# Kernel optimization log

Hardware: AMD Instinct MI355X
Metric: run time of the kernel (lower is better)

Reference implementation:

```python
import jax, jax.numpy as jnp
import numpy as np

N_ATOMS = 16384
N_EDGES = 524288
N_MOL = 256
A = 4            # num_pseudo_species
S = 4            # len(unique_numbers)
NMAX = 10        # radial basis size
NSPH = 9         # (l_max+1)^2 with l_max=2
Q = A * NMAX
NL = 3           # l_max+1
F = Q * Q * NL   # 4800 power-spectrum features
CUTOFF = 5.0
AVG_ATOMS = 64.0
SCALE = 1.0
H1, H2 = 512, 512


def _sph_l012(u):
    # real spherical harmonics l=0,1,2 on unit vectors u [E,3] -> [E,9]
    x, y, z = u[:, 0], u[:, 1], u[:, 2]
    c1 = 0.4886025119029199
    c2 = 1.0925484305920792
    return jnp.stack([
        jnp.full_like(x, 0.28209479177387814),
        c1 * y, c1 * z, c1 * x,
        c2 * x * y, c2 * y * z,
        0.31539156525252005 * (3.0 * z * z - 1.0),
        c2 * x * z,
        0.5462742152960396 * (x * x - y * y),
    ], axis=-1)


def _forward(positions, cells, edge_offsets, U, gamma, beta, W1, W2, W3, Wc,
             numbers, edge_indices, batch):
    send, recv = edge_indices[0], edge_indices[1]
    cell_e = cells[batch[send]]                                  # [E,3,3]
    rvec = positions[recv] - positions[send] + jnp.einsum('ek,ekl->el', edge_offsets, cell_e)
    r = jnp.sqrt(jnp.sum(rvec * rvec, axis=-1) + 1e-12)          # [E]
    rhat = rvec / r[:, None]
    fc = 0.5 * (jnp.cos(jnp.pi * r / CUTOFF) + 1.0) * (r < CUTOFF)
    mu = jnp.linspace(0.0, CUTOFF, NMAX)
    sig = CUTOFF / NMAX
    R = jnp.exp(-((r[:, None] - mu) ** 2) / (2.0 * sig * sig)) * fc[:, None]  # [E,NMAX]
    Y = _sph_l012(rhat)                                          # [E,9]
    RY = jnp.einsum('en,ek->enk', R, Y)                          # [E,NMAX,9]
    w = U[:, numbers[send]]                                      # [A,E] pseudo-species mix of neighbor species
    # spherical expansion per atom: c[i,a,n,lm]
    c = jnp.stack([jax.ops.segment_sum(w[a][:, None, None] * RY, recv, num_segments=N_ATOMS)
                   for a in range(A)], axis=1)                   # [N,A,NMAX,9]
    c = c.reshape(N_ATOMS, Q, NSPH)
    # power spectrum: contract over m within each l block, normalize by sqrt(2l+1)
    lblocks = [(0, 1, 1.0), (1, 4, 3.0), (4, 9, 5.0)]
    ps = jnp.stack([jnp.einsum('iqm,ipm->iqp', c[:, :, a:b], c[:, :, a:b]) / jnp.sqrt(nl)
                    for a, b, nl in lblocks], axis=-1).reshape(N_ATOMS, F)
    # layer norm
    mean = ps.mean(axis=-1, keepdims=True)
    var = ps.var(axis=-1, keepdims=True)
    x = (ps - mean) / jnp.sqrt(var + 1e-5) * gamma + beta

    def contract(x, W):
        # species-indexed contraction: per-species weight via combination matrix U
        Wsp = jnp.einsum('as,aio->sio', U, W)                    # [S,in,out]
        out = jnp.zeros((x.shape[0], W.shape[-1]), x.dtype)
        for s in range(S):                                       # small fixed species set
            out = out + jnp.where((numbers == s)[:, None], x @ Wsp[s], 0.0)
        return out

    x = jax.nn.silu(contract(x, W1))
    x = jax.nn.silu(contract(x, W2))
    x = contract(x, W3)                                          # [N,1]
    e = jax.ops.segment_sum(x, batch, num_segments=N_MOL)        # [M,1]
    e = e / jnp.sqrt(float(A)) / AVG_ATOMS
    comp = jax.ops.segment_sum(jax.nn.one_hot(numbers, S, dtype=x.dtype), batch, num_segments=N_MOL)
    return e * SCALE + comp @ Wc.T


def setup_inputs() -> dict:
    key = jax.random.key(0)
    ks = jax.random.split(key, 10)
    positions = jax.random.normal(ks[0], (N_ATOMS, 3), dtype=jnp.float32)
    cells = jnp.zeros((N_MOL, 3, 3), dtype=jnp.float32)
    numbers = jax.random.randint(ks[1], (N_ATOMS,), 0, S)
    edge_indices = jax.random.randint(ks[2], (2, N_EDGES), 0, N_ATOMS)
    edge_offsets = jnp.zeros((N_EDGES, 3), dtype=jnp.float32)
    batch = jnp.sort(jax.random.randint(ks[3], (N_ATOMS,), 0, N_MOL))
    U = jax.random.normal(ks[4], (A, S), dtype=jnp.float32) * 0.5
    gamma = jnp.ones((F,), dtype=jnp.float32)
    beta = jnp.zeros((F,), dtype=jnp.float32)
    W1 = jax.random.normal(ks[5], (A, F, H1), dtype=jnp.float32) / np.sqrt(F)
    W2 = jax.random.normal(ks[6], (A, H1, H2), dtype=jnp.float32) / np.sqrt(H1)
    W3 = jax.random.normal(ks[7], (A, H2, 1), dtype=jnp.float32) / np.sqrt(H2)
    Wc = jax.random.normal(ks[8], (1, S), dtype=jnp.float32) * 0.1
    return {"positions": positions, "cells": cells, "numbers": numbers,
            "edge_indices": edge_indices, "edge_offsets": edge_offsets, "batch": batch,
            "U": U, "gamma": gamma, "beta": beta, "W1": W1, "W2": W2, "W3": W3, "Wc": Wc}


def reference(positions, cells, numbers, edge_indices, edge_offsets, batch,
              U, gamma, beta, W1, W2, W3, Wc):
    return _forward(positions, cells, edge_offsets, U, gamma, beta, W1, W2, W3, Wc,
                    numbers, edge_indices, batch)
```

## Files before the change

kernel.cpp:

```cpp
#include <hip/hip_runtime.h>

#define NA   16384
#define NE   524288
#define NM   256
#define FF   4800
#define FR   2496
#define FL   832
#define NPAIR 820
#define HH   512
#define NMX  10
#define NSPH 9

typedef __bf16 bf16x8 __attribute__((ext_vector_type(8)));
typedef float  f32x4  __attribute__((ext_vector_type(4)));
typedef unsigned short u16x8 __attribute__((ext_vector_type(8)));

__device__ inline unsigned short f2bf(float x){
  unsigned int u = __builtin_bit_cast(unsigned int, x);
  u += 0x7fffu + ((u >> 16) & 1u);
  return (unsigned short)(u >> 16);
}
__device__ inline float bf2f(unsigned short h){
  unsigned int u = ((unsigned int)h) << 16;
  return __builtin_bit_cast(float, u);
}
__device__ inline void atomic_add_f(float* p, float v){
  __hip_atomic_fetch_add(p, v, __ATOMIC_RELAXED, __HIP_MEMORY_SCOPE_AGENT);
}
__device__ inline void gload16(const void* g, void* l){
  __builtin_amdgcn_global_load_lds(
      (const __attribute__((address_space(1))) unsigned int*)g,
      (__attribute__((address_space(3))) unsigned int*)l, 16, 0, 0);
}
__device__ inline float silu(float x){ return x / (1.f + __expf(-x)); }

__device__ inline void build_qp(unsigned short* qp, int tid){
  if (tid < 40){
    int q = tid;
    int m0 = q * 40 - (q * (q - 1)) / 2;
    for (int p = q; p < 40; p++) qp[m0 + p - q] = (unsigned short)((q << 8) | p);
  }
}

__device__ inline int block_scan_excl(int v, int tid, int* lds){
  int lane = tid & 63, w = tid >> 6;
  int x = v;
  #pragma unroll
  for (int d = 1; d < 64; d <<= 1){
    int y = __shfl_up(x, d, 64);
    if (lane >= d) x += y;
  }
  if (lane == 63) lds[w] = x;
  __syncthreads();
  int wsum = 0;
  for (int i = 0; i < w; i++) wsum += lds[i];
  return wsum + x - v;
}

__global__ __launch_bounds__(256) void k_hist(const int* __restrict__ ei,
                                              const int* __restrict__ numbers,
                                              int* __restrict__ cnt64k){
  int e = blockIdx.x * 256 + threadIdx.x;
  if (e < NE){
    int key = ei[NE + e] * 4 + numbers[ei[e]];
    atomicAdd(&cnt64k[key], 1);
  }
}

__global__ __launch_bounds__(256) void k_scanA(const int* __restrict__ cnt64k,
                                               int* __restrict__ bsum){
  __shared__ int lds[4];
  int tid = threadIdx.x;
  int v = cnt64k[blockIdx.x * 256 + tid];
  int lane = tid & 63;
  #pragma unroll
  for (int m = 32; m; m >>= 1) v += __shfl_xor(v, m, 64);
  if (lane == 0) lds[tid >> 6] = v;
  __syncthreads();
  if (tid == 0) bsum[blockIdx.x] = lds[0] + lds[1] + lds[2] + lds[3];
}

__global__ __launch_bounds__(256) void k_scanB(const int* __restrict__ bsum,
                                               int* __restrict__ boff, int* __restrict__ starts){
  __shared__ int lds[4];
  int tid = threadIdx.x;
  int v = bsum[tid];
  int e = block_scan_excl(v, tid, lds);
  boff[tid] = e;
  if (tid == 0) starts[65536] = NE;
}

__global__ __launch_bounds__(256) void k_scanC(const int* __restrict__ cnt64k,
                                               const int* __restrict__ boff,
                                               int* __restrict__ starts, int* __restrict__ cursor){
  __shared__ int lds[4];
  int tid = threadIdx.x;
  int bin = blockIdx.x * 256 + tid;
  int v = cnt64k[bin];
  int e = block_scan_excl(v, tid, lds) + boff[blockIdx.x];
  starts[bin] = e;
  cursor[bin] = e;
}

__global__ __launch_bounds__(256) void k_sortperm(const int* __restrict__ ei,
                                                  const int* __restrict__ numbers,
                                                  int* __restrict__ cursor, int* __restrict__ perm){
  int e = blockIdx.x * 256 + threadIdx.x;
  if (e < NE){
    int key = ei[NE + e] * 4 + numbers[ei[e]];
    int p = atomicAdd(&cursor[key], 1);
    perm[p] = e;
  }
}

__global__ __launch_bounds__(256) void k_acount(const int* __restrict__ numbers,
                                                int* __restrict__ bhist){
  __shared__ int h[4];
  int tid = threadIdx.x;
  if (tid < 4) h[tid] = 0;
  __syncthreads();
  atomicAdd(&h[numbers[blockIdx.x * 256 + tid]], 1);
  __syncthreads();
  if (tid < 4) bhist[blockIdx.x * 4 + tid] = h[tid];
}

__global__ void k_aoffs(const int* __restrict__ bhist, int* __restrict__ boffs,
                        int* __restrict__ ints){
  if (threadIdx.x == 0){
    int* cnt = ints; int* offs = ints + 8;
    int tot[4] = {0,0,0,0};
    for (int b = 0; b < 64; b++)
      for (int s = 0; s < 4; s++) tot[s] += bhist[b*4 + s];
    int o = 0;
    for (int s = 0; s < 4; s++){ cnt[s] = tot[s]; offs[s] = o; o += tot[s]; }
    offs[4] = o;
    int run[4];
    for (int s = 0; s < 4; s++) run[s] = offs[s];
    for (int b = 0; b < 64; b++)
      for (int s = 0; s < 4; s++){ boffs[b*4 + s] = run[s]; run[s] += bhist[b*4 + s]; }
  }
}

__global__ __launch_bounds__(256) void k_aplace(const int* __restrict__ numbers,
                                                const int* __restrict__ boffs,
                                                int* __restrict__ list){
  __shared__ int ws[4][4];
  int tid = threadIdx.x, w = tid >> 6, lane = tid & 63;
  int i = blockIdx.x * 256 + tid;
  int sp = numbers[i];
  int rank = 0;
  #pragma unroll
  for (int s = 0; s < 4; s++){
    unsigned long long m = __ballot(sp == s);
    if (s == sp) rank = __popcll(m & (((unsigned long long)1 << lane) - 1));
    if (lane == 0) ws[w][s] = __popcll(m);
  }
  __syncthreads();
  int pre = 0;
  for (int w2 = 0; w2 < w; w2++) pre += ws[w2][sp];
  list[boffs[blockIdx.x * 4 + sp] + pre + rank] = i;
}

__global__ __launch_bounds__(384) void k_atom(
    const float* __restrict__ pos, const float* __restrict__ cells,
    const int* __restrict__ ei, const float* __restrict__ eoff,
    const int* __restrict__ batch, const int* __restrict__ startsK,
    const int* __restrict__ perm, const float* __restrict__ U,
    unsigned short* __restrict__ ps, float* __restrict__ stats)
{
  __shared__ float Rl[64][NMX];
  __shared__ float Yl[64][NSPH];
  __shared__ float csr[360];
  __shared__ float cl[360];
  __shared__ float red[16];
  __shared__ float ul[16];
  __shared__ unsigned short qp[NPAIR];
  int atom = blockIdx.x;
  int tid = threadIdx.x;
  if (tid < 16) ul[tid] = U[tid];
  build_qp(qp, tid);
  int e0 = startsK[atom * 4], e1 = startsK[atom * 4 + 4];
  float px = pos[atom*3+0], py = pos[atom*3+1], pz = pos[atom*3+2];
  int sp = tid / 90, n = (tid % 90) / 9, k = tid % 9;
  int aS = 0, aE = 0;
  if (tid < 360){ aS = startsK[atom * 4 + sp]; aE = startsK[atom * 4 + sp + 1]; }
  float acc = 0.f;
  for (int base = e0; base < e1; base += 64){
    int nch = min(64, e1 - base);
    if (tid < nch){
      int e = perm[base + tid];
      int snd = ei[e];
      const float* C = cells + (size_t)batch[snd] * 9;
      float o0 = eoff[e*3+0], o1 = eoff[e*3+1], o2 = eoff[e*3+2];
      float rx = px - pos[snd*3+0] + o0*C[0] + o1*C[3] + o2*C[6];
      float ry = py - pos[snd*3+1] + o0*C[1] + o1*C[4] + o2*C[7];
      float rz = pz - pos[snd*3+2] + o0*C[2] + o1*C[5] + o2*C[8];
      float r = sqrtf(rx*rx + ry*ry + rz*rz + 1e-12f);
      float inv = 1.f / r;
      float hx = rx*inv, hy = ry*inv, hz = rz*inv;
      float fc = (r < 5.f) ? (0.5f * (__cosf(r * 0.6283185307179586f) + 1.f)) : 0.f;
      #pragma unroll
      for (int nn = 0; nn < NMX; nn++){
        float d = r - (5.f/9.f) * (float)nn;
        Rl[tid][nn] = __expf(-2.f * d * d) * fc;
      }
      Yl[tid][0] = 0.28209479177387814f;
      Yl[tid][1] = 0.4886025119029199f * hy;
      Yl[tid][2] = 0.4886025119029199f * hz;
      Yl[tid][3] = 0.4886025119029199f * hx;
      Yl[tid][4] = 1.0925484305920792f * hx * hy;
      Yl[tid][5] = 1.0925484305920792f * hy * hz;
      Yl[tid][6] = 0.31539156525252005f * (3.f * hz * hz - 1.f);
      Yl[tid][7] = 1.0925484305920792f * hx * hz;
      Yl[tid][8] = 0.5462742152960396f * (hx * hx - hy * hy);
    }
    __syncthreads();
    if (tid < 360){
      int lo2 = max(aS, base), hi2 = min(aE, base + nch);
      for (int e = lo2; e < hi2; e++){
        int j = e - base;
        acc += Rl[j][n] * Yl[j][k];
      }
    }
    __syncthreads();
  }
  if (tid < 360) csr[tid] = acc;
  __syncthreads();
  if (tid < 360){
    int a = tid / 90, nk = tid % 90;
    cl[tid] = ul[a*4+0]*csr[nk] + ul[a*4+1]*csr[90+nk]
            + ul[a*4+2]*csr[180+nk] + ul[a*4+3]*csr[270+nk];
  }
  __syncthreads();
  float s1 = 0.f, s2 = 0.f;
  if (tid < 312){
    int chunk = tid;
    int l = (chunk >= 208) ? 2 : ((chunk >= 104) ? 1 : 0);
    int m0 = (chunk - l * 104) * 8;
    unsigned short o[8];
    #pragma unroll
    for (int j = 0; j < 8; j++){
      int m = m0 + j;
      float v = 0.f, wgt = 0.f;
      if (m < NPAIR){
        int q = qp[m] >> 8, p = qp[m] & 255;
        const float* cq = &cl[q * 9];
        const float* cp = &cl[p * 9];
        if (l == 0)      v = cq[0]*cp[0];
        else if (l == 1) v = (cq[1]*cp[1] + cq[2]*cp[2] + cq[3]*cp[3]) * 0.5773502691896258f;
        else             v = (cq[4]*cp[4] + cq[5]*cp[5] + cq[6]*cp[6] + cq[7]*cp[7] + cq[8]*cp[8]) * 0.4472135954999579f;
        wgt = (p != q) ? 2.f : 1.f;
      }
      o[j] = f2bf(v);
      s1 += wgt * v; s2 += wgt * v * v;
    }
    *reinterpret_cast<u16x8*>(ps + (size_t)atom * FR + chunk * 8) = *(const u16x8*)o;
  }
  #pragma unroll
  for (int m = 32; m; m >>= 1){ s1 += __shfl_xor(s1, m, 64); s2 += __shfl_xor(s2, m, 64); }
  int w = tid >> 6, lane = tid & 63;
  if (lane == 0){ red[w] = s1; red[8 + w] = s2; }
  __syncthreads();
  if (tid == 0){
    float t1 = 0.f, t2 = 0.f;
    for (int i = 0; i < 6; i++){ t1 += red[i]; t2 += red[8 + i]; }
    float mean = t1 * (1.f / FF);
    float var = t2 * (1.f / FF) - mean * mean;
    var = fmaxf(var, 0.f);
    stats[2*atom]   = mean;
    stats[2*atom+1] = rsqrtf(var + 1e-5f);
  }
}

__global__ __launch_bounds__(256) void k_wg1(
    const float* __restrict__ W1, const float* __restrict__ U,
    const float* __restrict__ gamma, const float* __restrict__ beta,
    unsigned short* __restrict__ Wg, float* __restrict__ gW, float* __restrict__ bW)
{
  __shared__ float tg[64][65];
  __shared__ float tb[64][65];
  __shared__ unsigned short qp[NPAIR];
  int n0 = blockIdx.x * 64, f0 = blockIdx.y * 64, s = blockIdx.z;
  int l = blockIdx.y / 13;
  int mblk = (blockIdx.y - l * 13) * 64;
  float u0 = U[s], u1 = U[4+s], u2 = U[8+s], u3 = U[12+s];
  int tid = threadIdx.x;
  build_qp(qp, tid);
  __syncthreads();
  #pragma unroll 4
  for (int rep = 0; rep < 16; rep++){
    int idx = rep * 256 + tid;
    int fi = idx >> 6, ni = idx & 63;
    int m = mblk + fi;
    float tgv = 0.f, tbv = 0.f;
    if (m < NPAIR){
      int q = qp[m] >> 8, p = qp[m] & 255;
      int fa = (q * 40 + p) * 3 + l;
      size_t basea = (size_t)fa * 512 + (n0 + ni);
      float wa = u0*W1[basea] + u1*W1[basea + (size_t)FF*512]
               + u2*W1[basea + (size_t)2*FF*512] + u3*W1[basea + (size_t)3*FF*512];
      tgv = gamma[fa] * wa;
      tbv = beta[fa] * wa;
      if (p != q){
        int fb = (p * 40 + q) * 3 + l;
        size_t baseb = (size_t)fb * 512 + (n0 + ni);
        float wb = u0*W1[baseb] + u1*W1[baseb + (size_t)FF*512]
                 + u2*W1[baseb + (size_t)2*FF*512] + u3*W1[baseb + (size_t)3*FF*512];
        tgv += gamma[fb] * wb;
        tbv += beta[fb] * wb;
      }
    }
    tg[fi][ni] = tgv;
    tb[fi][ni] = tbv;
  }
  __syncthreads();
  #pragma unroll 4
  for (int rep = 0; rep < 16; rep++){
    int idx = rep * 256 + tid;
    int ni = idx >> 6, fi = idx & 63;
    Wg[((size_t)s * 512 + n0 + ni) * FR + f0 + fi] = f2bf(tg[fi][ni]);
  }
  if (tid < 64){
    float sg = 0.f, sb = 0.f;
    for (int fi = 0; fi < 64; fi++){ sg += tg[fi][tid]; sb += tb[fi][tid]; }
    atomic_add_f(&gW[s * 512 + n0 + tid], sg);
    atomic_add_f(&bW[s * 512 + n0 + tid], sb);
  }
}

__global__ __launch_bounds__(256) void k_w2t(
    const float* __restrict__ W2, const float* __restrict__ U,
    unsigned short* __restrict__ W2t)
{
  __shared__ float t[64][65];
  int n0 = blockIdx.x * 64, k0 = blockIdx.y * 64, s = blockIdx.z;
  float u0 = U[s], u1 = U[4+s], u2 = U[8+s], u3 = U[12+s];
  int tid = threadIdx.x;
  #pragma unroll 4
  for (int rep = 0; rep < 16; rep++){
    int idx = rep * 256 + tid;
    int ki = idx >> 6, ni = idx & 63;
    size_t base = (size_t)(k0 + ki) * 512 + (n0 + ni);
    t[ki][ni] = u0*W2[base] + u1*W2[base + 512*512]
              + u2*W2[base + 2*512*512] + u3*W2[base + 3*512*512];
  }
  __syncthreads();
  #pragma unroll 4
  for (int rep = 0; rep < 16; rep++){
    int idx = rep * 256 + tid;
    int ni = idx >> 6, ki = idx & 63;
    W2t[((size_t)s * 512 + n0 + ni) * 512 + k0 + ki] = f2bf(t[ki][ni]);
  }
}

__global__ void k_w3(const float* __restrict__ W3, const float* __restrict__ U,
                     float* __restrict__ W3s)
{
  int idx = blockIdx.x * 256 + threadIdx.x;
  if (idx < 4 * 512){
    int s = idx >> 9, k = idx & 511;
    W3s[idx] = U[s]*W3[k] + U[4+s]*W3[512+k] + U[8+s]*W3[2*512+k] + U[12+s]*W3[3*512+k];
  }
}

template<int EPI, int NSPLIT>
__global__ __launch_bounds__(256) void k_gemm(
    const unsigned short* __restrict__ Ag, int lda, int K,
    const unsigned short* __restrict__ Btg,
    const int* __restrict__ list, const int* __restrict__ offs, const int* __restrict__ cnt,
    unsigned short* __restrict__ pout,
    const float* __restrict__ W3s, float* __restrict__ pacc)
{
  __shared__ alignas(16) char smem[32768];
  const int NV = 4 * NSPLIT;
  int b = blockIdx.x;
  int y = (b & 7) + 8 * (b / (8 * NV));
  int v = (b >> 3) % NV;
  int x = v & 3, kh = v >> 2;

  int s = 0, t = y;
  for (; s < 4; s++){
    int nts = (cnt[s] + 127) >> 7;
    if (t < nts) break;
    t -= nts;
  }
  if (s >= 4) return;
  int cntS = cnt[s], offS = offs[s];
  int rt = t, n0 = x * 128;
  int tid = threadIdx.x, w = tid >> 6, lane = tid & 63;
  int wr = w >> 1, wc = w & 1;

  const unsigned short* Bts = Btg + (size_t)s * 512 * K;
  const unsigned short* gA[4];
  const unsigned short* gB[4];
  char* lA[4];
  char* lB[4];
  #pragma unroll
  for (int it = 0; it < 4; it++){
    int g = it * 4 + w;
    int idx = g * 64 + lane;
    int row = idx >> 3, ch = idx & 7;
    int cg = ch ^ (row & 7);
    int gr = rt * 128 + row; gr = gr < cntS ? gr : cntS - 1;
    int atom = list[offS + gr];
    gA[it] = Ag + (size_t)atom * lda + cg * 8;
    lA[it] = smem + g * 1024;
    gB[it] = Bts + (size_t)(n0 + row) * K + cg * 8;
    lB[it] = smem + 16384 + g * 1024;
  }

  int hi = lane >> 4, lo = lane & 15;
  f32x4 acc[4][4];
  #pragma unroll
  for (int mi = 0; mi < 4; mi++)
    #pragma unroll
    for (int ni = 0; ni < 4; ni++)
      #pragma unroll
      for (int r = 0; r < 4; r++) acc[mi][ni][r] = 0.f;

  int abase[4], a7[4], bbase[4], b7[4];
  #pragma unroll
  for (int mi = 0; mi < 4; mi++){ int row = wr*64 + mi*16 + lo; abase[mi] = row*128; a7[mi] = row & 7; }
  #pragma unroll
  for (int ni = 0; ni < 4; ni++){ int row = wc*64 + ni*16 + lo; bbase[ni] = 16384 + row*128; b7[ni] = row & 7; }

  int nk = K / 64;
  int k0 = ((nk * kh) / NSPLIT) * 64;
  int k1 = ((nk * (kh + 1)) / NSPLIT) * 64;

  for (int kt = k0; kt < k1; kt += 64){
    #pragma unroll
    for (int it = 0; it < 4; it++) gload16(gA[it] + kt, lA[it]);
    #pragma unroll
    for (int it = 0; it < 4; it++) gload16(gB[it] + kt, lB[it]);
    __syncthreads();
    #pragma unroll
    for (int kk = 0; kk < 2; kk++){
      bf16x8 af[4], bfr[4];
      #pragma unroll
      for (int mi = 0; mi < 4; mi++)
        af[mi] = *(const bf16x8*)(smem + abase[mi] + (((kk*4 + hi) ^ a7[mi]) << 4));
      #pragma unroll
      for (int ni = 0; ni < 4; ni++)
        bfr[ni] = *(const bf16x8*)(smem + bbase[ni] + (((kk*4 + hi) ^ b7[ni]) << 4));
      #pragma unroll
      for (int mi = 0; mi < 4; mi++)
        #pragma unroll
        for (int ni = 0; ni < 4; ni++)
          acc[mi][ni] = __builtin_amdgcn_mfma_f32_16x16x32_bf16(af[mi], bfr[ni], acc[mi][ni], 0, 0, 0);
    }
    __syncthreads();
  }

  int gn[4];
  #pragma unroll
  for (int ni = 0; ni < 4; ni++) gn[ni] = n0 + wc*64 + ni*16 + lo;

  if (EPI == 0){
    #pragma unroll
    for (int mi = 0; mi < 4; mi++){
      #pragma unroll
      for (int j = 0; j < 4; j++){
        int gr = rt*128 + wr*64 + mi*16 + hi*4 + j;
        if (gr < cntS){
          int atom = list[offS + gr];
          #pragma unroll
          for (int ni = 0; ni < 4; ni++)
            pout[((size_t)kh * NA + atom) * 512 + gn[ni]] = f2bf(acc[mi][ni][j]);
        }
      }
    }
  } else {
    float w3v[4];
    #pragma unroll
    for (int ni = 0; ni < 4; ni++) w3v[ni] = W3s[s * 512 + gn[ni]];
    float* pslot = pacc + (size_t)(x * 2 + wc) * NA;
    #pragma unroll
    for (int mi = 0; mi < 4; mi++){
      #pragma unroll
      for (int j = 0; j < 4; j++){
        int gr = rt*128 + wr*64 + mi*16 + hi*4 + j;
        if (gr < cntS){
          int atom = list[offS + gr];
          float pdot = 0.f;
          #pragma unroll
          for (int ni = 0; ni < 4; ni++)
            pdot += silu(acc[mi][ni][j]) * w3v[ni];
          pdot += __shfl_xor(pdot, 1, 16);
          pdot += __shfl_xor(pdot, 2, 16);
          pdot += __shfl_xor(pdot, 4, 16);
          pdot += __shfl_xor(pdot, 8, 16);
          if (lo == 0) pslot[atom] = pdot;
        }
      }
    }
  }
}

__global__ __launch_bounds__(256) void k_epi(
    const unsigned short* __restrict__ pbuf, const float* __restrict__ stats,
    const float* __restrict__ gW, const float* __restrict__ bW,
    const int* __restrict__ numbers, unsigned short* __restrict__ h1)
{
  int w = threadIdx.x >> 6, lane = threadIdx.x & 63;
  int atom = blockIdx.x * 4 + w;
  int s = numbers[atom];
  float mean = stats[2*atom], rstd = stats[2*atom+1];
  int c0 = lane * 8;
  u16x8 a0 = *reinterpret_cast<const u16x8*>(pbuf + (size_t)atom * 512 + c0);
  u16x8 a1 = *reinterpret_cast<const u16x8*>(pbuf + (size_t)(NA + atom) * 512 + c0);
  unsigned short o[8];
  #pragma unroll
  for (int j = 0; j < 8; j++){
    int c = c0 + j;
    float acc = bf2f(a0[j]) + bf2f(a1[j]);
    float vv = rstd * acc + bW[s*512 + c] - mean * rstd * gW[s*512 + c];
    o[j] = f2bf(silu(vv));
  }
  *reinterpret_cast<u16x8*>(h1 + (size_t)atom * 512 + c0) = *(const u16x8*)o;
}

__global__ __launch_bounds__(256) void k_final2(
    const float* __restrict__ pacc, const int* __restrict__ numbers,
    const int* __restrict__ batch, const float* __restrict__ Wc,
    float* __restrict__ molOut)
{
  int atom = blockIdx.x * 256 + threadIdx.x;
  int lane = threadIdx.x & 63;
  float sum = 0.f;
  #pragma unroll
  for (int p = 0; p < 8; p++) sum += pacc[(size_t)p * NA + atom];
  float val = sum * (1.f / 128.f) + Wc[numbers[atom]];
  int mol = batch[atom];
  int m0 = __shfl(mol, 0, 64);
  int m63 = __shfl(mol, 63, 64);
  if (m0 == m63){
    #pragma unroll
    for (int m = 32; m; m >>= 1) val += __shfl_xor(val, m, 64);
    if (lane == 0) atomic_add_f(&molOut[mol], val);
  } else {
    atomic_add_f(&molOut[mol], val);
  }
}

extern "C" void kernel_launch(void* const* d_in, const int* in_sizes, int n_in,
                              void* d_out, int out_size, void* d_ws, size_t ws_size,
                              hipStream_t stream)
{
  const float* pos     = (const float*)d_in[0];
  const float* cells   = (const float*)d_in[1];
  const int*   numbers = (const int*)d_in[2];
  const int*   ei      = (const int*)d_in[3];
  const float* eoff    = (const float*)d_in[4];
  const int*   batch   = (const int*)d_in[5];
  const float* U       = (const float*)d_in[6];
  const float* gamma   = (const float*)d_in[7];
  const float* beta    = (const float*)d_in[8];
  const float* W1      = (const float*)d_in[9];
  const float* W2      = (const float*)d_in[10];
  const float* W3      = (const float*)d_in[11];
  const float* Wc      = (const float*)d_in[12];
  float* out = (float*)d_out;

  char* ws = (char*)d_ws;
  size_t off = 0;
  auto alloc = [&](size_t bytes) -> void* {
    void* p = ws + off;
    off += (bytes + 255) & ~(size_t)255;
    return p;
  };
  unsigned short* ps   = (unsigned short*)alloc((size_t)NA * FR * 2);
  unsigned short* pbuf = (unsigned short*)alloc((size_t)2 * NA * 512 * 2);
  float* stats         = (float*)alloc((size_t)NA * 2 * 4);
  unsigned short* Wg1  = (unsigned short*)alloc((size_t)4 * 512 * FR * 2);
  float* gW            = (float*)alloc(4 * 512 * 4);
  float* bW            = (float*)alloc(4 * 512 * 4);
  unsigned short* W2t  = (unsigned short*)alloc((size_t)4 * 512 * 512 * 2);
  float* W3s           = (float*)alloc(4 * 512 * 4);
  unsigned short* h1   = (unsigned short*)alloc((size_t)NA * 512 * 2);
  float* pacc          = (float*)alloc((size_t)8 * NA * 4);
  int* list            = (int*)alloc(NA * 4);
  int* perm            = (int*)alloc((size_t)NE * 4);
  int* startsK         = (int*)alloc((65536 + 1) * 4);
  int* cnt64k          = (int*)alloc(65536 * 4);
  int* cursor64k       = (int*)alloc(65536 * 4);
  int* bsum            = (int*)alloc(256 * 4);
  int* boff            = (int*)alloc(256 * 4);
  int* bhist           = (int*)alloc(64 * 4 * 4);
  int* boffs           = (int*)alloc(64 * 4 * 4);
  int* ints            = (int*)alloc(64);
  int* cnt = ints; int* offs = ints + 8;

  hipMemsetAsync(cnt64k, 0, 65536 * 4, stream);
  hipMemsetAsync(gW, 0, 4 * 512 * 4, stream);
  hipMemsetAsync(bW, 0, 4 * 512 * 4, stream);
  hipMemsetAsync(out, 0, (size_t)out_size * 4, stream);

  k_hist<<<NE / 256, 256, 0, stream>>>(ei, numbers, cnt64k);
  k_scanA<<<256, 256, 0, stream>>>(cnt64k, bsum);
  k_scanB<<<1, 256, 0, stream>>>(bsum, boff, startsK);
  k_scanC<<<256, 256, 0, stream>>>(cnt64k, boff, startsK, cursor64k);
  k_sortperm<<<NE / 256, 256, 0, stream>>>(ei, numbers, cursor64k, perm);

  k_acount<<<NA / 256, 256, 0, stream>>>(numbers, bhist);
  k_aoffs<<<1, 64, 0, stream>>>(bhist, boffs, ints);
  k_aplace<<<NA / 256, 256, 0, stream>>>(numbers, boffs, list);

  k_atom<<<NA, 384, 0, stream>>>(pos, cells, ei, eoff, batch, startsK, perm, U, ps, stats);

  k_wg1<<<dim3(8, 39, 4), 256, 0, stream>>>(W1, U, gamma, beta, Wg1, gW, bW);
  k_w2t<<<dim3(8, 8, 4), 256, 0, stream>>>(W2, U, W2t);
  k_w3<<<8, 256, 0, stream>>>(W3, U, W3s);

  k_gemm<0, 2><<<1088, 256, 0, stream>>>(ps, FR, FR, Wg1, list, offs, cnt,
                                         pbuf, nullptr, nullptr);
  k_epi<<<NA / 4, 256, 0, stream>>>(pbuf, stats, gW, bW, numbers, h1);

  k_gemm<2, 1><<<544, 256, 0, stream>>>(h1, 512, 512, W2t, list, offs, cnt,
                                        nullptr, W3s, pacc);
  k_final2<<<NA / 256, 256, 0, stream>>>(pacc, numbers, batch, Wc, out);
}
```

Baseline: 334.6 us.

## Split edge geometry into separate fully-parallel kernel writing SoA edge features

Moves per-edge geometry (distance, radial basis, spherical harmonics) out of the per-atom kernel into a dedicated kernel that uses all threads and writes a 19-channel structure-of-arrays buffer in sorted edge order. The per-atom kernel then loads these channels with coalesced reads into shared memory instead of having only up to 64 of its 384 threads compute edges serially with scattered gathers. In exchange it adds an extra launch and roughly 40 MB of global write-plus-read traffic for the intermediate buffer.

New measurement: 361.3 us, median of 2. 1.08x slower.

```diff
diff --git a/kernel.cpp b/kernel.cpp
--- a/kernel.cpp
+++ b/kernel.cpp
@@ -161,15 +161,47 @@
   list[boffs[blockIdx.x * 4 + sp] + pre + rank] = i;
 }
 
-__global__ __launch_bounds__(384) void k_atom(
+__global__ __launch_bounds__(256) void k_egeom(
     const float* __restrict__ pos, const float* __restrict__ cells,
     const int* __restrict__ ei, const float* __restrict__ eoff,
-    const int* __restrict__ batch, const int* __restrict__ startsK,
-    const int* __restrict__ perm, const float* __restrict__ U,
+    const int* __restrict__ batch, const int* __restrict__ perm,
+    float* __restrict__ ef)
+{
+  int i = blockIdx.x * 256 + threadIdx.x;
+  if (i >= NE) return;
+  int e = perm[i];
+  int snd = ei[e], rcv = ei[NE + e];
+  const float* C = cells + (size_t)batch[snd] * 9;
+  float o0 = eoff[e*3+0], o1 = eoff[e*3+1], o2 = eoff[e*3+2];
+  float rx = pos[rcv*3+0] - pos[snd*3+0] + o0*C[0] + o1*C[3] + o2*C[6];
+  float ry = pos[rcv*3+1] - pos[snd*3+1] + o0*C[1] + o1*C[4] + o2*C[7];
+  float rz = pos[rcv*3+2] - pos[snd*3+2] + o0*C[2] + o1*C[5] + o2*C[8];
+  float r = sqrtf(rx*rx + ry*ry + rz*rz + 1e-12f);
+  float inv = 1.f / r;
+  float hx = rx*inv, hy = ry*inv, hz = rz*inv;
+  float fc = (r < 5.f) ? (0.5f * (__cosf(r * 0.6283185307179586f) + 1.f)) : 0.f;
+  #pragma unroll
+  for (int nn = 0; nn < NMX; nn++){
+    float d = r - (5.f/9.f) * (float)nn;
+    ef[(size_t)nn * NE + i] = __expf(-2.f * d * d) * fc;
+  }
+  ef[(size_t)10 * NE + i] = 0.28209479177387814f;
+  ef[(size_t)11 * NE + i] = 0.4886025119029199f * hy;
+  ef[(size_t)12 * NE + i] = 0.4886025119029199f * hz;
+  ef[(size_t)13 * NE + i] = 0.4886025119029199f * hx;
+  ef[(size_t)14 * NE + i] = 1.0925484305920792f * hx * hy;
+  ef[(size_t)15 * NE + i] = 1.0925484305920792f * hy * hz;
+  ef[(size_t)16 * NE + i] = 0.31539156525252005f * (3.f * hz * hz - 1.f);
+  ef[(size_t)17 * NE + i] = 1.0925484305920792f * hx * hz;
+  ef[(size_t)18 * NE + i] = 0.5462742152960396f * (hx * hx - hy * hy);
+}
+
+__global__ __launch_bounds__(384) void k_atom2(
+    const float* __restrict__ ef, const int* __restrict__ startsK,
+    const float* __restrict__ U,
     unsigned short* __restrict__ ps, float* __restrict__ stats)
 {
-  __shared__ float Rl[64][NMX];
-  __shared__ float Yl[64][NSPH];
+  __shared__ float efl[64][21];
   __shared__ float csr[360];
   __shared__ float cl[360];
   __shared__ float red[16];
@@ -180,46 +212,24 @@
   if (tid < 16) ul[tid] = U[tid];
   build_qp(qp, tid);
   int e0 = startsK[atom * 4], e1 = startsK[atom * 4 + 4];
-  float px = pos[atom*3+0], py = pos[atom*3+1], pz = pos[atom*3+2];
   int sp = tid / 90, n = (tid % 90) / 9, k = tid % 9;
   int aS = 0, aE = 0;
   if (tid < 360){ aS = startsK[atom * 4 + sp]; aE = startsK[atom * 4 + sp + 1]; }
   float acc = 0.f;
   for (int base = e0; base < e1; base += 64){
     int nch = min(64, e1 - base);
-    if (tid < nch){
-      int e = perm[base + tid];
-      int snd = ei[e];
-      const float* C = cells + (size_t)batch[snd] * 9;
-      float o0 = eoff[e*3+0], o1 = eoff[e*3+1], o2 = eoff[e*3+2];
-      float rx = px - pos[snd*3+0] + o0*C[0] + o1*C[3] + o2*C[6];
-      float ry = py - pos[snd*3+1] + o0*C[1] + o1*C[4] + o2*C[7];
-      float rz = pz - pos[snd*3+2] + o0*C[2] + o1*C[5] + o2*C[8];
-      float r = sqrtf(rx*rx + ry*ry + rz*rz + 1e-12f);
-      float inv = 1.f / r;
-      float hx = rx*inv, hy = ry*inv, hz = rz*inv;
-      float fc = (r < 5.f) ? (0.5f * (__cosf(r * 0.6283185307179586f) + 1.f)) : 0.f;
-      #pragma unroll
-      for (int nn = 0; nn < NMX; nn++){
-        float d = r - (5.f/9.f) * (float)nn;
-        Rl[tid][nn] = __expf(-2.f * d * d) * fc;
-      }
-      Yl[tid][0] = 0.28209479177387814f;
-      Yl[tid][1] = 0.4886025119029199f * hy;
-      Yl[tid][2] = 0.4886025119029199f * hz;
-      Yl[tid][3] = 0.4886025119029199f * hx;
-      Yl[tid][4] = 1.0925484305920792f * hx * hy;
-      Yl[tid][5] = 1.0925484305920792f * hy * hz;
-      Yl[tid][6] = 0.31539156525252005f * (3.f * hz * hz - 1.f);
-      Yl[tid][7] = 1.0925484305920792f * hx * hz;
-      Yl[tid][8] = 0.5462742152960396f * (hx * hx - hy * hy);
+    for (int idx = tid; idx < 19 * 64; idx += 384){
+      int j = idx >> 6, ln = idx & 63;
+      float v = 0.f;
+      if (ln < nch) v = ef[(size_t)j * NE + base + ln];
+      efl[ln][j] = v;
     }
     __syncthreads();
     if (tid < 360){
       int lo2 = max(aS, base), hi2 = min(aE, base + nch);
       for (int e = lo2; e < hi2; e++){
         int j = e - base;
-        acc += Rl[j][n] * Yl[j][k];
+        acc += efl[j][n] * efl[j][10 + k];
       }
     }
     __syncthreads();
@@ -570,6 +580,7 @@
     return p;
   };
   unsigned short* ps   = (unsigned short*)alloc((size_t)NA * FR * 2);
+  float* ef            = (float*)alloc((size_t)19 * NE * 4);
   unsigned short* pbuf = (unsigned short*)alloc((size_t)2 * NA * 512 * 2);
   float* stats         = (float*)alloc((size_t)NA * 2 * 4);
   unsigned short* Wg1  = (unsigned short*)alloc((size_t)4 * 512 * FR * 2);
@@ -606,7 +617,8 @@
   k_aoffs<<<1, 64, 0, stream>>>(bhist, boffs, ints);
   k_aplace<<<NA / 256, 256, 0, stream>>>(numbers, boffs, list);
 
-  k_atom<<<NA, 384, 0, stream>>>(pos, cells, ei, eoff, batch, startsK, perm, U, ps, stats);
+  k_egeom<<<NE / 256, 256, 0, stream>>>(pos, cells, ei, eoff, batch, perm, ef);
+  k_atom2<<<NA, 384, 0, stream>>>(ef, startsK, U, ps, stats);
 
   k_wg1<<<dim3(8, 39, 4), 256, 0, stream>>>(W1, U, gamma, beta, Wg1, gW, bW);
   k_w2t<<<dim3(8, 8, 4), 256, 0, stream>>>(W2, U, W2t);
```

## Interleave power-spectrum l-blocks per pair and restructure atom and weight-prep kernels

Applied to the files above, without the earlier changes.

The power-spectrum feature layout moves from l-major blocks to pair-major with the three l values interleaved. Each of 104 threads now computes all three l contractions for 8 pairs and caches the q-row coefficients, instead of 312 threads each doing one l. The atom kernel widens to 512 threads with 128-edge chunks and aligns species groups to 128-thread slots. The W1 preparation kernel is rewritten to read W1 once per species-mix across all 4 output species, and the transposed bf16 output is staged in shared memory with vector stores. This cuts redundant W1 reads and edge-chunk iterations, at the cost of idle threads in the atom kernel.

Result: slower. 358.8 us (+7.2%).

```diff
diff --git a/kernel.cpp b/kernel.cpp
--- a/kernel.cpp
+++ b/kernel.cpp
@@ -5,7 +5,6 @@
 #define NM   256
 #define FF   4800
 #define FR   2496
-#define FL   832
 #define NPAIR 820
 #define HH   512
 #define NMX  10
@@ -161,15 +160,15 @@
   list[boffs[blockIdx.x * 4 + sp] + pre + rank] = i;
 }
 
-__global__ __launch_bounds__(384) void k_atom(
+__global__ __launch_bounds__(512) void k_atom3(
     const float* __restrict__ pos, const float* __restrict__ cells,
     const int* __restrict__ ei, const float* __restrict__ eoff,
     const int* __restrict__ batch, const int* __restrict__ startsK,
     const int* __restrict__ perm, const float* __restrict__ U,
     unsigned short* __restrict__ ps, float* __restrict__ stats)
 {
-  __shared__ float Rl[64][NMX];
-  __shared__ float Yl[64][NSPH];
+  __shared__ float Rl[128][NMX];
+  __shared__ float Yl[128][NSPH];
   __shared__ float csr[360];
   __shared__ float cl[360];
   __shared__ float red[16];
@@ -181,12 +180,12 @@
   build_qp(qp, tid);
   int e0 = startsK[atom * 4], e1 = startsK[atom * 4 + 4];
   float px = pos[atom*3+0], py = pos[atom*3+1], pz = pos[atom*3+2];
-  int sp = tid / 90, n = (tid % 90) / 9, k = tid % 9;
-  int aS = 0, aE = 0;
-  if (tid < 360){ aS = startsK[atom * 4 + sp]; aE = startsK[atom * 4 + sp + 1]; }
+  int sp = tid >> 7, nk = tid & 127;
+  int n = nk / 9, k = nk - n * 9;
+  int aS = startsK[atom * 4 + sp], aE = startsK[atom * 4 + sp + 1];
   float acc = 0.f;
-  for (int base = e0; base < e1; base += 64){
-    int nch = min(64, e1 - base);
+  for (int base = e0; base < e1; base += 128){
+    int nch = min(128, e1 - base);
     if (tid < nch){
       int e = perm[base + tid];
       int snd = ei[e];
@@ -215,7 +214,7 @@
       Yl[tid][8] = 0.5462742152960396f * (hx * hx - hy * hy);
     }
     __syncthreads();
-    if (tid < 360){
+    if (nk < 90){
       int lo2 = max(aS, base), hi2 = min(aE, base + nch);
       for (int e = lo2; e < hi2; e++){
         int j = e - base;
@@ -224,37 +223,47 @@
     }
     __syncthreads();
   }
-  if (tid < 360) csr[tid] = acc;
+  if (nk < 90) csr[sp * 90 + nk] = acc;
   __syncthreads();
   if (tid < 360){
-    int a = tid / 90, nk = tid % 90;
-    cl[tid] = ul[a*4+0]*csr[nk] + ul[a*4+1]*csr[90+nk]
-            + ul[a*4+2]*csr[180+nk] + ul[a*4+3]*csr[270+nk];
+    int a = tid / 90, nq = tid % 90;
+    cl[tid] = ul[a*4+0]*csr[nq] + ul[a*4+1]*csr[90+nq]
+            + ul[a*4+2]*csr[180+nq] + ul[a*4+3]*csr[270+nq];
   }
   __syncthreads();
   float s1 = 0.f, s2 = 0.f;
-  if (tid < 312){
-    int chunk = tid;
-    int l = (chunk >= 208) ? 2 : ((chunk >= 104) ? 1 : 0);
-    int m0 = (chunk - l * 104) * 8;
-    unsigned short o[8];
+  if (tid < 104){
+    unsigned short ob[24];
+    int qc = -1;
+    float cq0=0,cq1=0,cq2=0,cq3=0,cq4=0,cq5=0,cq6=0,cq7=0,cq8=0;
     #pragma unroll
     for (int j = 0; j < 8; j++){
-      int m = m0 + j;
-      float v = 0.f, wgt = 0.f;
+      int m = tid * 8 + j;
+      float v0 = 0.f, v1 = 0.f, v2 = 0.f, wgt = 0.f;
       if (m < NPAIR){
         int q = qp[m] >> 8, p = qp[m] & 255;
-        const float* cq = &cl[q * 9];
+        if (q != qc){
+          const float* c = &cl[q * 9];
+          cq0=c[0]; cq1=c[1]; cq2=c[2]; cq3=c[3]; cq4=c[4];
+          cq5=c[5]; cq6=c[6]; cq7=c[7]; cq8=c[8];
+          qc = q;
+        }
         const float* cp = &cl[p * 9];
-        if (l == 0)      v = cq[0]*cp[0];
-        else if (l == 1) v = (cq[1]*cp[1] + cq[2]*cp[2] + cq[3]*cp[3]) * 0.5773502691896258f;
-        else             v = (cq[4]*cp[4] + cq[5]*cp[5] + cq[6]*cp[6] + cq[7]*cp[7] + cq[8]*cp[8]) * 0.4472135954999579f;
+        v0 = cq0 * cp[0];
+        v1 = (cq1*cp[1] + cq2*cp[2] + cq3*cp[3]) * 0.5773502691896258f;
+        v2 = (cq4*cp[4] + cq5*cp[5] + cq6*cp[6] + cq7*cp[7] + cq8*cp[8]) * 0.4472135954999579f;
         wgt = (p != q) ? 2.f : 1.f;
       }
-      o[j] = f2bf(v);
-      s1 += wgt * v; s2 += wgt * v * v;
-    }
-    *reinterpret_cast<u16x8*>(ps + (size_t)atom * FR + chunk * 8) = *(const u16x8*)o;
+      ob[j*3+0] = f2bf(v0);
+      ob[j*3+1] = f2bf(v1);
+      ob[j*3+2] = f2bf(v2);
+      s1 += wgt * (v0 + v1 + v2);
+      s2 += wgt * (v0*v0 + v1*v1 + v2*v2);
+    }
+    unsigned short* dst = ps + (size_t)atom * FR + tid * 24;
+    *reinterpret_cast<u16x8*>(dst)      = *(const u16x8*)&ob[0];
+    *reinterpret_cast<u16x8*>(dst + 8)  = *(const u16x8*)&ob[8];
+    *reinterpret_cast<u16x8*>(dst + 16) = *(const u16x8*)&ob[16];
   }
   #pragma unroll
   for (int m = 32; m; m >>= 1){ s1 += __shfl_xor(s1, m, 64); s2 += __shfl_xor(s2, m, 64); }
@@ -262,8 +271,8 @@
   if (lane == 0){ red[w] = s1; red[8 + w] = s2; }
   __syncthreads();
   if (tid == 0){
-    float t1 = 0.f, t2 = 0.f;
-    for (int i = 0; i < 6; i++){ t1 += red[i]; t2 += red[8 + i]; }
+    float t1 = red[0] + red[1];
+    float t2 = red[8] + red[9];
     float mean = t1 * (1.f / FF);
     float var = t2 * (1.f / FF) - mean * mean;
     var = fmaxf(var, 0.f);
@@ -272,59 +281,64 @@
   }
 }
 
-__global__ __launch_bounds__(256) void k_wg1(
+__global__ __launch_bounds__(256) void k_wg2(
     const float* __restrict__ W1, const float* __restrict__ U,
     const float* __restrict__ gamma, const float* __restrict__ beta,
     unsigned short* __restrict__ Wg, float* __restrict__ gW, float* __restrict__ bW)
 {
-  __shared__ float tg[64][65];
-  __shared__ float tb[64][65];
+  __shared__ unsigned short og[4][64][96];
   __shared__ unsigned short qp[NPAIR];
-  int n0 = blockIdx.x * 64, f0 = blockIdx.y * 64, s = blockIdx.z;
-  int l = blockIdx.y / 13;
-  int mblk = (blockIdx.y - l * 13) * 64;
-  float u0 = U[s], u1 = U[4+s], u2 = U[8+s], u3 = U[12+s];
-  int tid = threadIdx.x;
+  int n0 = blockIdx.x * 64, m0 = blockIdx.y * 32;
+  int tid = threadIdx.x, pl = tid >> 6, nn = tid & 63;
   build_qp(qp, tid);
-  __syncthreads();
-  #pragma unroll 4
-  for (int rep = 0; rep < 16; rep++){
-    int idx = rep * 256 + tid;
-    int fi = idx >> 6, ni = idx & 63;
-    int m = mblk + fi;
-    float tgv = 0.f, tbv = 0.f;
+  float u[4][4];
+  #pragma unroll
+  for (int a = 0; a < 4; a++)
+    #pragma unroll
+    for (int s = 0; s < 4; s++) u[a][s] = U[a*4 + s];
+  __syncthreads();
+  float gs[4] = {0,0,0,0}, bs[4] = {0,0,0,0};
+  for (int it = 0; it < 24; it++){
+    int plc = it * 4 + pl;
+    int m = m0 + plc / 3, l = plc % 3;
+    float tg[4] = {0,0,0,0}, tb[4] = {0,0,0,0};
     if (m < NPAIR){
       int q = qp[m] >> 8, p = qp[m] & 255;
       int fa = (q * 40 + p) * 3 + l;
-      size_t basea = (size_t)fa * 512 + (n0 + ni);
-      float wa = u0*W1[basea] + u1*W1[basea + (size_t)FF*512]
-               + u2*W1[basea + (size_t)2*FF*512] + u3*W1[basea + (size_t)3*FF*512];
-      tgv = gamma[fa] * wa;
-      tbv = beta[fa] * wa;
-      if (p != q){
-        int fb = (p * 40 + q) * 3 + l;
-        size_t baseb = (size_t)fb * 512 + (n0 + ni);
-        float wb = u0*W1[baseb] + u1*W1[baseb + (size_t)FF*512]
-                 + u2*W1[baseb + (size_t)2*FF*512] + u3*W1[baseb + (size_t)3*FF*512];
-        tgv += gamma[fb] * wb;
-        tbv += beta[fb] * wb;
+      float ga = gamma[fa], ba = beta[fa];
+      float gb = 0.f, bb = 0.f;
+      int fb = fa;
+      if (p != q){ fb = (p * 40 + q) * 3 + l; gb = gamma[fb]; bb = beta[fb]; }
+      #pragma unroll
+      for (int a = 0; a < 4; a++){
+        float wa = W1[(size_t)a * FF * 512 + (size_t)fa * 512 + n0 + nn];
+        float wb = (p != q) ? W1[(size_t)a * FF * 512 + (size_t)fb * 512 + n0 + nn] : 0.f;
+        float gf = ga * wa + gb * wb;
+        float bf = ba * wa + bb * wb;
+        #pragma unroll
+        for (int s = 0; s < 4; s++){
+          tg[s] += u[a][s] * gf;
+          tb[s] += u[a][s] * bf;
+        }
       }
     }
-    tg[fi][ni] = tgv;
-    tb[fi][ni] = tbv;
-  }
-  __syncthreads();
-  #pragma unroll 4
-  for (int rep = 0; rep < 16; rep++){
-    int idx = rep * 256 + tid;
-    int ni = idx >> 6, fi = idx & 63;
-    Wg[((size_t)s * 512 + n0 + ni) * FR + f0 + fi] = f2bf(tg[fi][ni]);
-  }
-  if (tid < 64){
-    float sg = 0.f, sb = 0.f;
-    for (int fi = 0; fi < 64; fi++){ sg += tg[fi][tid]; sb += tb[fi][tid]; }
-    atomic_add_f(&gW[s * 512 + n0 + tid], sg);
-    atomic_add_f(&bW[s * 512 + n0 + tid], sb);
+    #pragma unroll
+    for (int s = 0; s < 4; s++){
+      og[s][nn][plc] = f2bf(tg[s]);
+      gs[s] += tg[s];
+      bs[s] += tb[s];
+    }
+  }
+  #pragma unroll
+  for (int s = 0; s < 4; s++){
+    atomic_add_f(&gW[s * 512 + n0 + nn], gs[s]);
+    atomic_add_f(&bW[s * 512 + n0 + nn], bs[s]);
+  }
+  __syncthreads();
+  for (int idx = tid; idx < 4 * 64 * 12; idx += 256){
+    int c8 = idx % 12; int sn = idx / 12; int s = sn >> 6, nnn = sn & 63;
+    u16x8 v = *reinterpret_cast<const u16x8*>(&og[s][nnn][c8 * 8]);
+    *reinterpret_cast<u16x8*>(&Wg[((size_t)s * 512 + n0 + nnn) * FR + 3 * m0 + c8 * 8]) = v;
   }
 }
 
@@ -606,9 +620,9 @@
   k_aoffs<<<1, 64, 0, stream>>>(bhist, boffs, ints);
   k_aplace<<<NA / 256, 256, 0, stream>>>(numbers, boffs, list);
 
-  k_atom<<<NA, 384, 0, stream>>>(pos, cells, ei, eoff, batch, startsK, perm, U, ps, stats);
-
-  k_wg1<<<dim3(8, 39, 4), 256, 0, stream>>>(W1, U, gamma, beta, Wg1, gW, bW);
+  k_atom3<<<NA, 512, 0, stream>>>(pos, cells, ei, eoff, batch, startsK, perm, U, ps, stats);
+
+  k_wg2<<<dim3(8, 26), 256, 0, stream>>>(W1, U, gamma, beta, Wg1, gW, bW);
   k_w2t<<<dim3(8, 8, 4), 256, 0, stream>>>(W2, U, W2t);
   k_w3<<<8, 256, 0, stream>>>(W3, U, W3s);
 
```

## Reorganize power-spectrum features into 4x4 q/p blocks per l

Applied to the files above, without the earlier changes.

Changes the reduced power-spectrum feature layout from a flat upper-triangle pair list per l into 55 blocks of 4x4 (q,p) tiles, each holding all three l values. Each thread now computes a 4x4 tile, reusing register-loaded coefficient vectors and dropping the qp lookup table in k_atom and k_wg1. The row width grows from 2496 to 2688 padded features, including zeroed lower-triangle entries in diagonal blocks, so the first GEMM's K dimension and the ps buffer both get larger.

Result: no change. 331.4 us (-1.0%).

```diff
diff --git a/kernel.cpp b/kernel.cpp
--- a/kernel.cpp
+++ b/kernel.cpp
@@ -4,9 +4,7 @@
 #define NE   524288
 #define NM   256
 #define FF   4800
-#define FR   2496
-#define FL   832
-#define NPAIR 820
+#define FR   2688
 #define HH   512
 #define NMX  10
 #define NSPH 9
@@ -34,12 +32,38 @@
 }
 __device__ inline float silu(float x){ return x / (1.f + __expf(-x)); }
 
-__device__ inline void build_qp(unsigned short* qp, int tid){
-  if (tid < 40){
-    int q = tid;
-    int m0 = q * 40 - (q * (q - 1)) / 2;
-    for (int p = q; p < 40; p++) qp[m0 + p - q] = (unsigned short)((q << 8) | p);
-  }
+__device__ inline void decode_blk(int b, int& qb, int& pb){
+  int q = 0, rem = b;
+  while (rem >= 10 - q){ rem -= 10 - q; q++; }
+  qb = q; pb = q + rem;
+}
+
+template<int CNT>
+__device__ inline void ps_block(const float* __restrict__ cl, int qb, int pb, int off,
+                                float nrm, bool diag, unsigned short* ob,
+                                float& s1, float& s2){
+  float cq[4][CNT], cp[4][CNT];
+  #pragma unroll
+  for (int i = 0; i < 4; i++)
+    #pragma unroll
+    for (int k = 0; k < CNT; k++){
+      cq[i][k] = cl[(qb*4 + i)*9 + off + k];
+      cp[i][k] = cl[(pb*4 + i)*9 + off + k];
+    }
+  #pragma unroll
+  for (int qi = 0; qi < 4; qi++)
+    #pragma unroll
+    for (int pi = 0; pi < 4; pi++){
+      float v = 0.f;
+      #pragma unroll
+      for (int k = 0; k < CNT; k++) v += cq[qi][k] * cp[pi][k];
+      v *= nrm;
+      float wgt = diag ? ((qi < pi) ? 2.f : ((qi == pi) ? 1.f : 0.f)) : 2.f;
+      if (diag && qi > pi) v = 0.f;
+      ob[qi*4 + pi] = f2bf(v);
+      s1 += wgt * v;
+      s2 += wgt * v * v;
+    }
 }
 
 __device__ inline int block_scan_excl(int v, int tid, int* lds){
@@ -174,11 +198,9 @@
   __shared__ float cl[360];
   __shared__ float red[16];
   __shared__ float ul[16];
-  __shared__ unsigned short qp[NPAIR];
   int atom = blockIdx.x;
   int tid = threadIdx.x;
   if (tid < 16) ul[tid] = U[tid];
-  build_qp(qp, tid);
   int e0 = startsK[atom * 4], e1 = startsK[atom * 4 + 4];
   float px = pos[atom*3+0], py = pos[atom*3+1], pz = pos[atom*3+2];
   int sp = tid / 90, n = (tid % 90) / 9, k = tid % 9;
@@ -233,28 +255,21 @@
   }
   __syncthreads();
   float s1 = 0.f, s2 = 0.f;
-  if (tid < 312){
-    int chunk = tid;
-    int l = (chunk >= 208) ? 2 : ((chunk >= 104) ? 1 : 0);
-    int m0 = (chunk - l * 104) * 8;
-    unsigned short o[8];
-    #pragma unroll
-    for (int j = 0; j < 8; j++){
-      int m = m0 + j;
-      float v = 0.f, wgt = 0.f;
-      if (m < NPAIR){
-        int q = qp[m] >> 8, p = qp[m] & 255;
-        const float* cq = &cl[q * 9];
-        const float* cp = &cl[p * 9];
-        if (l == 0)      v = cq[0]*cp[0];
-        else if (l == 1) v = (cq[1]*cp[1] + cq[2]*cp[2] + cq[3]*cp[3]) * 0.5773502691896258f;
-        else             v = (cq[4]*cp[4] + cq[5]*cp[5] + cq[6]*cp[6] + cq[7]*cp[7] + cq[8]*cp[8]) * 0.4472135954999579f;
-        wgt = (p != q) ? 2.f : 1.f;
-      }
-      o[j] = f2bf(v);
-      s1 += wgt * v; s2 += wgt * v * v;
-    }
-    *reinterpret_cast<u16x8*>(ps + (size_t)atom * FR + chunk * 8) = *(const u16x8*)o;
+  int l = tid >> 6, b = tid & 63;
+  if (l < 3 && b < 55){
+    int qb, pb;
+    decode_blk(b, qb, pb);
+    bool diag = (qb == pb);
+    unsigned short ob[16];
+    if (l == 0)      ps_block<1>(cl, qb, pb, 0, 1.f, diag, ob, s1, s2);
+    else if (l == 1) ps_block<3>(cl, qb, pb, 1, 0.5773502691896258f, diag, ob, s1, s2);
+    else             ps_block<5>(cl, qb, pb, 4, 0.4472135954999579f, diag, ob, s1, s2);
+    unsigned short* dst = ps + (size_t)atom * FR + b * 48 + l * 16;
+    *reinterpret_cast<u16x8*>(dst)     = *(const u16x8*)&ob[0];
+    *reinterpret_cast<u16x8*>(dst + 8) = *(const u16x8*)&ob[8];
+  } else if (tid >= 192 && tid < 198){
+    unsigned short zb[8] = {0,0,0,0,0,0,0,0};
+    *reinterpret_cast<u16x8*>(ps + (size_t)atom * FR + 2640 + (tid - 192) * 8) = *(const u16x8*)zb;
   }
   #pragma unroll
   for (int m = 32; m; m >>= 1){ s1 += __shfl_xor(s1, m, 64); s2 += __shfl_xor(s2, m, 64); }
@@ -279,35 +294,37 @@
 {
   __shared__ float tg[64][65];
   __shared__ float tb[64][65];
-  __shared__ unsigned short qp[NPAIR];
   int n0 = blockIdx.x * 64, f0 = blockIdx.y * 64, s = blockIdx.z;
-  int l = blockIdx.y / 13;
-  int mblk = (blockIdx.y - l * 13) * 64;
   float u0 = U[s], u1 = U[4+s], u2 = U[8+s], u3 = U[12+s];
   int tid = threadIdx.x;
-  build_qp(qp, tid);
-  __syncthreads();
   #pragma unroll 4
   for (int rep = 0; rep < 16; rep++){
     int idx = rep * 256 + tid;
     int fi = idx >> 6, ni = idx & 63;
-    int m = mblk + fi;
+    int fp = f0 + fi;
+    int b = fp / 48, r = fp % 48;
+    int l = r >> 4, qi = (r >> 2) & 3, pi = r & 3;
     float tgv = 0.f, tbv = 0.f;
-    if (m < NPAIR){
-      int q = qp[m] >> 8, p = qp[m] & 255;
-      int fa = (q * 40 + p) * 3 + l;
-      size_t basea = (size_t)fa * 512 + (n0 + ni);
-      float wa = u0*W1[basea] + u1*W1[basea + (size_t)FF*512]
-               + u2*W1[basea + (size_t)2*FF*512] + u3*W1[basea + (size_t)3*FF*512];
-      tgv = gamma[fa] * wa;
-      tbv = beta[fa] * wa;
-      if (p != q){
-        int fb = (p * 40 + q) * 3 + l;
-        size_t baseb = (size_t)fb * 512 + (n0 + ni);
-        float wb = u0*W1[baseb] + u1*W1[baseb + (size_t)FF*512]
-                 + u2*W1[baseb + (size_t)2*FF*512] + u3*W1[baseb + (size_t)3*FF*512];
-        tgv += gamma[fb] * wb;
-        tbv += beta[fb] * wb;
+    if (b < 55){
+      int qb, pb;
+      decode_blk(b, qb, pb);
+      bool zero = (qb == pb) && (qi > pi);
+      if (!zero){
+        int q = qb*4 + qi, p = pb*4 + pi;
+        int fa = (q * 40 + p) * 3 + l;
+        size_t basea = (size_t)fa * 512 + (n0 + ni);
+        float wa = u0*W1[basea] + u1*W1[basea + (size_t)FF*512]
+                 + u2*W1[basea + (size_t)2*FF*512] + u3*W1[basea + (size_t)3*FF*512];
+        tgv = gamma[fa] * wa;
+        tbv = beta[fa] * wa;
+        if (p != q){
+          int fb = (p * 40 + q) * 3 + l;
+          size_t baseb = (size_t)fb * 512 + (n0 + ni);
+          float wb = u0*W1[baseb] + u1*W1[baseb + (size_t)FF*512]
+                   + u2*W1[baseb + (size_t)2*FF*512] + u3*W1[baseb + (size_t)3*FF*512];
+          tgv += gamma[fb] * wb;
+          tbv += beta[fb] * wb;
+        }
       }
     }
     tg[fi][ni] = tgv;
@@ -608,7 +625,7 @@
 
   k_atom<<<NA, 384, 0, stream>>>(pos, cells, ei, eoff, batch, startsK, perm, U, ps, stats);
 
-  k_wg1<<<dim3(8, 39, 4), 256, 0, stream>>>(W1, U, gamma, beta, Wg1, gW, bW);
+  k_wg1<<<dim3(8, 42, 4), 256, 0, stream>>>(W1, U, gamma, beta, Wg1, gW, bW);
   k_w2t<<<dim3(8, 8, 4), 256, 0, stream>>>(W2, U, W2t);
   k_w3<<<8, 256, 0, stream>>>(W3, U, W3s);
 
```
